# Performance work log

Hardware: AMD Instinct MI355X
Metric: run time of the kernel (lower is better)

Reference implementation:

```python
import jax, jax.numpy as jnp
import numpy as np
import math

KH, KW = 3, 3
CIN, COUT = 48, 48
H, W = 128, 128
DELTA = 0.001


def _gabor_weights(freq, theta, sigma, psi, f0, theta0):
    # grids exactly as in torch __init__: x0 = ceil(kh/2), linspace(-x0+1, x0, kh)
    x0 = math.ceil(KH / 2)
    y0 = math.ceil(KW / 2)
    ly = jnp.linspace(-x0 + 1.0, float(x0), KH)
    lx = jnp.linspace(-y0 + 1.0, float(y0), KW)
    Y, X = jnp.meshgrid(ly, lx, indexing='ij')  # [kh,kw], Y varies on dim0
    # broadcast per-(out,in) scalars over the kernel grid -> [O,I,kh,kw]
    th = theta[:, :, None, None]
    sg = sigma[:, :, None, None]
    fr = freq[:, :, None, None]
    ps = psi[:, :, None, None]
    F0 = f0[:, :, None, None]
    th0 = theta0[:, :, None, None]
    rotx = X * jnp.cos(th) + Y * jnp.sin(th)
    roty = -X * jnp.sin(th) + Y * jnp.cos(th)
    r = jnp.sqrt(rotx ** 2 + roty ** 2 + DELTA)
    g_radial = jnp.exp(-((jnp.log(r) - jnp.log(F0)) / (2.0 * jnp.log(sg / F0))) ** 2)
    g_angular = jnp.exp(-(th - th0) ** 2 / (2.0 * sg ** 2))
    g = g_radial * g_angular * jnp.cos(fr * r + ps)
    g = g / (2.0 * math.pi * sg ** 2)
    return g  # [O,I,KH,KW]


def setup_inputs() -> dict:
    key = jax.random.key(0)
    ks = jax.random.split(key, 5)
    pi = math.pi
    return {
        'x': jax.random.normal(ks[0], (1, CIN, H, W), dtype=jnp.float32),
        'freq': jax.random.uniform(ks[1], (COUT, CIN), dtype=jnp.float32) * pi,
        'theta': jax.random.uniform(ks[2], (COUT, CIN), dtype=jnp.float32) * pi,
        'sigma': jax.random.uniform(ks[3], (COUT, CIN), dtype=jnp.float32) * pi,
        'psi': jax.random.uniform(ks[4], (COUT, CIN), dtype=jnp.float32) * pi,
        'f0': jnp.ones((COUT, CIN), dtype=jnp.float32),
        'theta0': jnp.ones((COUT, CIN), dtype=jnp.float32),
    }


def reference(x, freq, theta, sigma, psi, f0, theta0):
    w = _gabor_weights(freq, theta, sigma, psi, f0, theta0)  # [O,I,kh,kw]
    # frequency-domain filtering: fft2(x) [1,I,H,W] * fft2(w, s=(H,W)) [O,I,H,W]
    x_freq = jnp.fft.fft2(x)
    w_freq = jnp.fft.fft2(w, s=(H, W))
    xf = x_freq * w_freq  # broadcast (B=1) -> [O,I,H,W]
    crow, ccol = H // 2, W // 2
    mask = jnp.zeros((H, W), dtype=x.dtype).at[crow - 30:crow + 30, ccol - 30:ccol + 30].set(1.0)
    x_filtered = jnp.fft.ifft2(xf * mask).real  # [O,I,H,W]
    out = jax.lax.conv_general_dilated(
        x_filtered, w,
        window_strides=(1, 1), padding=[(1, 1), (1, 1)],
        dimension_numbers=('NCHW', 'OIHW', 'NCHW'))
    return out  # [O,O,H,W]
```

## Files before the change

kernel.cpp:

```cpp
#include <hip/hip_runtime.h>

#define CIN 48
#define COUT 48
#define NPIX 16384

typedef float f32x4 __attribute__((ext_vector_type(4)));
typedef short bf16x8 __attribute__((ext_vector_type(8)));

__device__ __forceinline__ unsigned short f2bf(float f) {
  unsigned u = __float_as_uint(f);
  unsigned r = (u + 0x7FFFu + ((u >> 16) & 1u)) >> 16;
  return (unsigned short)r;
}

__global__ __launch_bounds__(256) void gabor_k(
    const float* __restrict__ freq, const float* __restrict__ theta,
    const float* __restrict__ sigma, const float* __restrict__ psi,
    const float* __restrict__ f0, const float* __restrict__ theta0,
    float* __restrict__ wout, unsigned short* __restrict__ wbf64)
{
  int idx = blockIdx.x * 256 + threadIdx.x;
  if (idx < 432 * 16) {
    wbf64[(idx >> 4) * 64 + 48 + (idx & 15)] = 0;
  }
  if (idx >= COUT * CIN * 9) return;
  int k = idx % 9;
  int oi = idx / 9;
  int oc = oi / CIN, ic = oi % CIN;
  int a = k / 3, b = k % 3;
  float Yv = (a == 0) ? -1.0f : ((a == 1) ? 0.5f : 2.0f);
  float Xv = (b == 0) ? -1.0f : ((b == 1) ? 0.5f : 2.0f);
  float th = theta[oi], sg = sigma[oi], fr = freq[oi], ps = psi[oi];
  float F0 = f0[oi], th0 = theta0[oi];
  float c = cosf(th), s = sinf(th);
  float rotx =  Xv * c + Yv * s;
  float roty = -Xv * s + Yv * c;
  float r = sqrtf(rotx * rotx + roty * roty + 0.001f);
  float denom = 2.0f * logf(sg / F0);
  float t1 = (logf(r) - logf(F0)) / denom;
  float g_rad = expf(-t1 * t1);
  float dth = th - th0;
  float g_ang = expf(-dth * dth / (2.0f * sg * sg));
  float g = g_rad * g_ang * cosf(fr * r + ps) / (6.283185307179586f * sg * sg);
  wout[idx] = g;
  wbf64[(k * 48 + oc) * 64 + ic] = f2bf(g);
}

__global__ void circ_k(float* __restrict__ ar, float* __restrict__ ai)
{
  int d = threadIdx.x;
  float sr = 0.f, si = 0.f;
  for (int u = 34; u < 94; ++u) {
    int m = (u * d) & 127;
    float ang = (float)m * 0.049087385212340526f;
    sr += cosf(ang);
    si += sinf(ang);
  }
  ar[d] = sr * (1.0f / 128.0f);
  ai[d] = si * (1.0f / 128.0f);
}

__global__ __launch_bounds__(256) void stage1_k(
    const float* __restrict__ x, const float* __restrict__ arr,
    const float* __restrict__ aii, float2* __restrict__ Up)
{
  __shared__ float Xs[16 * 128];
  __shared__ float ars[128], ais[128];
  int yg = blockIdx.x, i = blockIdx.y;
  int t = threadIdx.x;
  const float* Xi = x + i * NPIX + yg * 16 * 128;
  for (int p = t; p < 2048; p += 256) Xs[p] = Xi[p];
  if (t < 128) { ars[t] = arr[t]; ais[t] = aii[t]; }
  __syncthreads();
  int j = t & 127;
  int ysl = t >> 7;
  float accr[8], acci[8];
#pragma unroll
  for (int yy = 0; yy < 8; ++yy) { accr[yy] = 0.f; acci[yy] = 0.f; }
  for (int xx = 0; xx < 128; ++xx) {
    float tr = ars[(j - xx) & 127];
    float ti = ais[(j - xx) & 127];
#pragma unroll
    for (int yy = 0; yy < 8; ++yy) {
      float xv = Xs[(ysl * 8 + yy) * 128 + xx];
      accr[yy] += xv * tr;
      acci[yy] += xv * ti;
    }
  }
  float2* UpI = Up + i * NPIX;
  int ybase = yg * 16 + ysl * 8;
#pragma unroll
  for (int yy = 0; yy < 8; ++yy)
    UpI[(ybase + yy) * 128 + j] = make_float2(accr[yy], acci[yy]);
}

__global__ __launch_bounds__(256) void stage2_k(
    const float2* __restrict__ Up, const float* __restrict__ arr,
    const float* __restrict__ aii, float* __restrict__ yf)
{
  __shared__ float2 Us[128 * 16];
  __shared__ float ars[128], ais[128];
  int jg = blockIdx.x, i = blockIdx.y;
  int t = threadIdx.x;
  const float2* UpI = Up + i * NPIX;
  for (int p = t; p < 2048; p += 256) {
    int y = p >> 4, jj = p & 15;
    Us[p] = UpI[y * 128 + jg * 16 + jj];
  }
  if (t < 128) { ars[t] = arr[t]; ais[t] = aii[t]; }
  __syncthreads();
  int yp = t & 127;
  int xsl = t >> 7;
  float acc[8];
#pragma unroll
  for (int xx = 0; xx < 8; ++xx) acc[xx] = 0.f;
  for (int y = 0; y < 128; ++y) {
    float tr = ars[(yp - y) & 127];
    float ti = ais[(yp - y) & 127];
#pragma unroll
    for (int xx = 0; xx < 8; ++xx) {
      float2 u = Us[y * 16 + xsl * 8 + xx];
      acc[xx] += u.x * tr - u.y * ti;
    }
  }
  float* yfI = yf + i * NPIX;
  int xb = jg * 16 + xsl * 8;
#pragma unroll
  for (int xx = 0; xx < 8; ++xx)
    yfI[yp * 128 + xb + xx] = acc[xx];
}

__global__ __launch_bounds__(256, 3) void conv2_k(
    const float* __restrict__ yf, const float* __restrict__ wts,
    const unsigned short* __restrict__ wbf64, float* __restrict__ out)
{
  __shared__ __align__(16) short XF[324 * 56 + 16];

  int o  = blockIdx.z;
  int y0 = blockIdx.y * 16, x0 = blockIdx.x * 16;
  int tid = threadIdx.x;

  for (int p = tid; p < 324; p += 256)
    *(bf16x8*)(XF + p * 56 + 48) = (bf16x8){0,0,0,0,0,0,0,0};
  if (tid < 16) XF[324 * 56 + tid] = 0;

  if (tid < 240) {
    int s = tid;
    int i = s / 5, sp = s - i * 5;
    const float* Wp = wts + (o * CIN + i) * 9;
    float W0 = Wp[0], W1 = Wp[1], W2 = Wp[2], W3 = Wp[3], W4 = Wp[4],
          W5 = Wp[5], W6 = Wp[6], W7 = Wp[7], W8 = Wp[8];
    const float* yfp = yf + i * NPIX;
    int cb = (x0 - 4 + 4 * sp) & 127;
    float Ra[8], Rb[8], Rc[8];

#define LOADROW(dst, ry) { \
    const float* rp_ = yfp + (((ry) & 127) << 7); \
    float2 q0_ = *(const float2*)(rp_ + cb); \
    float2 q1_ = *(const float2*)(rp_ + ((cb + 2) & 127)); \
    float2 q2_ = *(const float2*)(rp_ + ((cb + 4) & 127)); \
    float2 q3_ = *(const float2*)(rp_ + ((cb + 6) & 127)); \
    dst[0]=q0_.x; dst[1]=q0_.y; dst[2]=q1_.x; dst[3]=q1_.y; \
    dst[4]=q2_.x; dst[5]=q2_.y; dst[6]=q3_.x; dst[7]=q3_.y; }

#define EMIT(rr, R2_, R1_, R0_) { \
    int y_ = y0 - 1 + (rr); \
    bool yok_ = (y_ >= 0) && (y_ < 128); \
    _Pragma("unroll") \
    for (int j = 0; j < 4; ++j) { \
      int cidx_ = 4 * sp + j; \
      if (cidx_ < 18) { \
        int xg_ = x0 - 1 + cidx_; \
        float v_ = 0.f; \
        if (yok_ && xg_ >= 0 && xg_ < 128) { \
          v_ = W0 * R0_[j + 3] + W1 * R0_[j + 2] + W2 * R0_[j + 1] \
             + W3 * R1_[j + 3] + W4 * R1_[j + 2] + W5 * R1_[j + 1] \
             + W6 * R2_[j + 3] + W7 * R2_[j + 2] + W8 * R2_[j + 1]; \
        } \
        XF[((rr) * 18 + cidx_) * 56 + i] = (short)f2bf(v_); \
      } } }

    LOADROW(Ra, y0 - 3)
    LOADROW(Rb, y0 - 2)
#pragma unroll
    for (int rr = 0; rr < 18; rr += 3) {
      LOADROW(Rc, y0 - 1 + rr)  EMIT(rr,     Ra, Rb, Rc)
      LOADROW(Ra, y0 + rr)      EMIT(rr + 1, Rb, Rc, Ra)
      LOADROW(Rb, y0 + 1 + rr)  EMIT(rr + 2, Rc, Ra, Rb)
    }
#undef LOADROW
#undef EMIT
  }
  __syncthreads();

  int wv = tid >> 6, lane = tid & 63;
  int tx = lane & 15, gq = lane >> 4;
  f32x4 acc[4][3];
#pragma unroll
  for (int nn = 0; nn < 4; ++nn)
#pragma unroll
    for (int m = 0; m < 3; ++m) acc[nn][m] = (f32x4){0.f, 0.f, 0.f, 0.f};

  const unsigned short* abase = wbf64 + (tx)*64;
  bf16x8 Ac0[3], Ac1[3], An0[3], An1[3];
#pragma unroll
  for (int m = 0; m < 3; ++m) {
    const unsigned short* ap = abase + (0 * 48 + m * 16) * 64;
    Ac0[m] = *(const bf16x8*)(ap + gq * 8);
    Ac1[m] = *(const bf16x8*)(ap + 32 + gq * 8);
  }

  for (int k = 0; k < 9; ++k) {
    if (k < 8) {
#pragma unroll
      for (int m = 0; m < 3; ++m) {
        const unsigned short* ap = abase + ((k + 1) * 48 + m * 16) * 64;
        An0[m] = *(const bf16x8*)(ap + gq * 8);
        An1[m] = *(const bf16x8*)(ap + 32 + gq * 8);
      }
    }
    int dy = k / 3, dx = k - dy * 3;
#pragma unroll
    for (int nn = 0; nn < 4; ++nn) {
      int n = wv * 4 + nn;
      const short* bp = XF + ((n + dy) * 18 + tx + dx) * 56;
      bf16x8 B0 = *(const bf16x8*)(bp + gq * 8);
      bf16x8 B1 = *(const bf16x8*)(bp + 32 + gq * 8);
#pragma unroll
      for (int m = 0; m < 3; ++m) {
        acc[nn][m] = __builtin_amdgcn_mfma_f32_16x16x32_bf16(Ac0[m], B0, acc[nn][m], 0, 0, 0);
        acc[nn][m] = __builtin_amdgcn_mfma_f32_16x16x32_bf16(Ac1[m], B1, acc[nn][m], 0, 0, 0);
      }
    }
#pragma unroll
    for (int m = 0; m < 3; ++m) { Ac0[m] = An0[m]; Ac1[m] = An1[m]; }
  }

#pragma unroll
  for (int nn = 0; nn < 4; ++nn) {
    int y = y0 + wv * 4 + nn;
#pragma unroll
    for (int m = 0; m < 3; ++m) {
#pragma unroll
      for (int r = 0; r < 4; ++r) {
        int oc = m * 16 + gq * 4 + r;
        out[((size_t)(o * COUT + oc) << 14) + (y << 7) + x0 + tx] = acc[nn][m][r];
      }
    }
  }
}

extern "C" void kernel_launch(void* const* d_in, const int* in_sizes, int n_in,
                              void* d_out, int out_size, void* d_ws, size_t ws_size,
                              hipStream_t stream)
{
  const float* x      = (const float*)d_in[0];
  const float* freq   = (const float*)d_in[1];
  const float* theta  = (const float*)d_in[2];
  const float* sigma  = (const float*)d_in[3];
  const float* psi    = (const float*)d_in[4];
  const float* f0     = (const float*)d_in[5];
  const float* theta0 = (const float*)d_in[6];
  float* out = (float*)d_out;
  float* ws  = (float*)d_ws;

  float*  w   = ws;
  float*  ar  = ws + 20736;
  float*  ai  = ws + 20864;
  float2* Up  = (float2*)(ws + 21248);
  float*  yf  = ws + 21248 + CIN * NPIX * 2;
  unsigned short* wbf64 = (unsigned short*)(ws + 21248 + CIN * NPIX * 3);

  gabor_k<<<dim3(81), dim3(256), 0, stream>>>(freq, theta, sigma, psi, f0, theta0, w, wbf64);
  circ_k<<<dim3(1), dim3(128), 0, stream>>>(ar, ai);
  stage1_k<<<dim3(8, 48), dim3(256), 0, stream>>>(x, ar, ai, Up);
  stage2_k<<<dim3(8, 48), dim3(256), 0, stream>>>(Up, ar, ai, yf);
  conv2_k<<<dim3(8, 8, 48), dim3(256), 0, stream>>>(yf, w, wbf64, out);
}
```

Baseline: 184.2 us.

## Shrink LDS tile and drop A prefetch to raise conv2 occupancy

The conv2 kernel's shared tile stride drops from 56 to 48 shorts and the per-pixel zero padding is removed. The padded weight columns (zero in channels 48-63) cancel the neighbouring pixel data the 64-wide B reads now pick up. The register double-buffer for the A weights is replaced by per-iteration loads, and launch bounds move from 3 to 5 blocks per SM. The pre-filter stage is split over 480 tasks using all 256 threads, with float4 row loads. The aim is higher occupancy and better producer parallelism. The costs are possible LDS bank conflicts at the 96-byte stride and exposed A-load latency.

```diff
diff --git a/kernel.cpp b/kernel.cpp
--- a/kernel.cpp
+++ b/kernel.cpp
@@ -130,38 +130,35 @@
     yfI[yp * 128 + xb + xx] = acc[xx];
 }
 
-__global__ __launch_bounds__(256, 3) void conv2_k(
+__global__ __launch_bounds__(256, 5) void conv2_k(
     const float* __restrict__ yf, const float* __restrict__ wts,
     const unsigned short* __restrict__ wbf64, float* __restrict__ out)
 {
-  __shared__ __align__(16) short XF[324 * 56 + 16];
+  __shared__ __align__(16) short XF[324 * 48 + 32];
 
   int o  = blockIdx.z;
   int y0 = blockIdx.y * 16, x0 = blockIdx.x * 16;
   int tid = threadIdx.x;
 
-  for (int p = tid; p < 324; p += 256)
-    *(bf16x8*)(XF + p * 56 + 48) = (bf16x8){0,0,0,0,0,0,0,0};
-  if (tid < 16) XF[324 * 56 + tid] = 0;
-
-  if (tid < 240) {
-    int s = tid;
-    int i = s / 5, sp = s - i * 5;
+  if (tid < 32) XF[324 * 48 + tid] = 0;
+
+  for (int s = tid; s < 480; s += 256) {
+    int i = s / 10, r10 = s - i * 10;
+    int sp = r10 % 5, half = r10 / 5;
     const float* Wp = wts + (o * CIN + i) * 9;
     float W0 = Wp[0], W1 = Wp[1], W2 = Wp[2], W3 = Wp[3], W4 = Wp[4],
           W5 = Wp[5], W6 = Wp[6], W7 = Wp[7], W8 = Wp[8];
     const float* yfp = yf + i * NPIX;
     int cb = (x0 - 4 + 4 * sp) & 127;
+    int rbase = half * 9;
     float Ra[8], Rb[8], Rc[8];
 
 #define LOADROW(dst, ry) { \
     const float* rp_ = yfp + (((ry) & 127) << 7); \
-    float2 q0_ = *(const float2*)(rp_ + cb); \
-    float2 q1_ = *(const float2*)(rp_ + ((cb + 2) & 127)); \
-    float2 q2_ = *(const float2*)(rp_ + ((cb + 4) & 127)); \
-    float2 q3_ = *(const float2*)(rp_ + ((cb + 6) & 127)); \
-    dst[0]=q0_.x; dst[1]=q0_.y; dst[2]=q1_.x; dst[3]=q1_.y; \
-    dst[4]=q2_.x; dst[5]=q2_.y; dst[6]=q3_.x; dst[7]=q3_.y; }
+    float4 q0_ = *(const float4*)(rp_ + cb); \
+    float4 q1_ = *(const float4*)(rp_ + ((cb + 4) & 127)); \
+    dst[0]=q0_.x; dst[1]=q0_.y; dst[2]=q0_.z; dst[3]=q0_.w; \
+    dst[4]=q1_.x; dst[5]=q1_.y; dst[6]=q1_.z; dst[7]=q1_.w; }
 
 #define EMIT(rr, R2_, R1_, R0_) { \
     int y_ = y0 - 1 + (rr); \
@@ -177,13 +174,14 @@
              + W3 * R1_[j + 3] + W4 * R1_[j + 2] + W5 * R1_[j + 1] \
              + W6 * R2_[j + 3] + W7 * R2_[j + 2] + W8 * R2_[j + 1]; \
         } \
-        XF[((rr) * 18 + cidx_) * 56 + i] = (short)f2bf(v_); \
+        XF[((rr) * 18 + cidx_) * 48 + i] = (short)f2bf(v_); \
       } } }
 
-    LOADROW(Ra, y0 - 3)
-    LOADROW(Rb, y0 - 2)
-#pragma unroll
-    for (int rr = 0; rr < 18; rr += 3) {
+    LOADROW(Ra, y0 - 3 + rbase)
+    LOADROW(Rb, y0 - 2 + rbase)
+#pragma unroll
+    for (int rr0 = 0; rr0 < 9; rr0 += 3) {
+      int rr = rbase + rr0;
       LOADROW(Rc, y0 - 1 + rr)  EMIT(rr,     Ra, Rb, Rc)
       LOADROW(Ra, y0 + rr)      EMIT(rr + 1, Rb, Rc, Ra)
       LOADROW(Rb, y0 + 1 + rr)  EMIT(rr + 2, Rc, Ra, Rb)
@@ -202,28 +200,20 @@
     for (int m = 0; m < 3; ++m) acc[nn][m] = (f32x4){0.f, 0.f, 0.f, 0.f};
 
   const unsigned short* abase = wbf64 + (tx)*64;
-  bf16x8 Ac0[3], Ac1[3], An0[3], An1[3];
-#pragma unroll
-  for (int m = 0; m < 3; ++m) {
-    const unsigned short* ap = abase + (0 * 48 + m * 16) * 64;
-    Ac0[m] = *(const bf16x8*)(ap + gq * 8);
-    Ac1[m] = *(const bf16x8*)(ap + 32 + gq * 8);
-  }
 
   for (int k = 0; k < 9; ++k) {
-    if (k < 8) {
-#pragma unroll
-      for (int m = 0; m < 3; ++m) {
-        const unsigned short* ap = abase + ((k + 1) * 48 + m * 16) * 64;
-        An0[m] = *(const bf16x8*)(ap + gq * 8);
-        An1[m] = *(const bf16x8*)(ap + 32 + gq * 8);
-      }
+    bf16x8 Ac0[3], Ac1[3];
+#pragma unroll
+    for (int m = 0; m < 3; ++m) {
+      const unsigned short* ap = abase + (k * 48 + m * 16) * 64;
+      Ac0[m] = *(const bf16x8*)(ap + gq * 8);
+      Ac1[m] = *(const bf16x8*)(ap + 32 + gq * 8);
     }
     int dy = k / 3, dx = k - dy * 3;
 #pragma unroll
     for (int nn = 0; nn < 4; ++nn) {
       int n = wv * 4 + nn;
-      const short* bp = XF + ((n + dy) * 18 + tx + dx) * 56;
+      const short* bp = XF + ((n + dy) * 18 + tx + dx) * 48;
       bf16x8 B0 = *(const bf16x8*)(bp + gq * 8);
       bf16x8 B1 = *(const bf16x8*)(bp + 32 + gq * 8);
 #pragma unroll
@@ -232,8 +222,6 @@
         acc[nn][m] = __builtin_amdgcn_mfma_f32_16x16x32_bf16(Ac1[m], B1, acc[nn][m], 0, 0, 0);
       }
     }
-#pragma unroll
-    for (int m = 0; m < 3; ++m) { Ac0[m] = An0[m]; Ac1[m] = An1[m]; }
   }
 
 #pragma unroll
```

Measured after the change: 329.0 us. +78.6%, slower.
